# Performance work log

Measured on AMD Instinct MI355X. Metric: run time of the kernel, lower is better.

The kernel has to match this reference:

```python
import jax, jax.numpy as jnp
import numpy as np

W_LEN, BSZ, EMBED, NHEADS = 1024, 16, 512, 8
HEAD_DIM = EMBED // NHEADS
LN_EPS = 1e-5


def setup_inputs() -> dict:
    key = jax.random.key(0)
    ks = jax.random.split(key, 7)
    s = 1.0 / np.sqrt(EMBED)
    return {
        "feat": jax.random.normal(ks[0], (W_LEN, BSZ, EMBED), dtype=jnp.float32),
        "in_proj_w": jax.random.normal(ks[1], (3 * EMBED, EMBED), dtype=jnp.float32) * s,
        "in_proj_b": jax.random.normal(ks[2], (3 * EMBED,), dtype=jnp.float32) * 0.02,
        "out_w": jax.random.normal(ks[3], (EMBED, EMBED), dtype=jnp.float32) * s,
        "out_b": jax.random.normal(ks[4], (EMBED,), dtype=jnp.float32) * 0.02,
        "ln_g": jnp.ones((EMBED,), dtype=jnp.float32),
        "ln_b": jnp.zeros((EMBED,), dtype=jnp.float32),
    }


def _layernorm(x, g, b):
    mu = jnp.mean(x, axis=-1, keepdims=True)
    var = jnp.mean(jnp.square(x - mu), axis=-1, keepdims=True)
    return (x - mu) * jax.lax.rsqrt(var + LN_EPS) * g + b


def reference(feat, in_proj_w, in_proj_b, out_w, out_b, ln_g, ln_b):
    w, bsz, embed = feat.shape
    x = _layernorm(feat, ln_g, ln_b)
    # fused qkv projection (self-attention branch of the torch code)
    qkv = x @ in_proj_w.T + in_proj_b                      # [w, b, 3E]
    q, k, v = jnp.split(qkv, 3, axis=-1)
    scaling = float(HEAD_DIM) ** -0.5
    q = (q * scaling).reshape(w, bsz, NHEADS, HEAD_DIM)
    k = k.reshape(w, bsz, NHEADS, HEAD_DIM)
    v = v.reshape(w, bsz, NHEADS, HEAD_DIM)
    # scores [b, h, w, w2]
    attn = jnp.einsum('wnhd,vnhd->nhwv', q, k)
    attn = jax.nn.softmax(attn, axis=-1)
    v_out = jnp.einsum('nhwv,vnhd->wnhd', attn, v).reshape(w, bsz, embed)
    v_out = v_out @ out_w.T + out_b
    return feat + v_out
```

## Files before the change

### kernel.cpp

```cpp
#include <hip/hip_runtime.h>
#include <math.h>

#define W_LEN 1024
#define BSZ 16
#define EMBED 512
#define NHEADS 8
#define HEAD_DIM 64
#define TOKENS (W_LEN * BSZ)
#define LN_EPS 1e-5f

typedef __bf16 bf16_t;
typedef bf16_t bf16x8 __attribute__((ext_vector_type(8)));
typedef float f32x4 __attribute__((ext_vector_type(4)));

__device__ inline unsigned short f2bf(float f) {
    unsigned int u = __float_as_uint(f);
    u += 0x7fffu + ((u >> 16) & 1u);
    return (unsigned short)(u >> 16);
}

__device__ __forceinline__ void async16(const void* g, void* l) {
    __builtin_amdgcn_global_load_lds(
        (__attribute__((address_space(1))) void*)g,
        (__attribute__((address_space(3))) void*)l, 16, 0, 0);
}

__global__ __launch_bounds__(256) void cvt_f32_bf16(const float* __restrict__ src,
                                                    unsigned short* __restrict__ dst) {
    int i = (blockIdx.x * 256 + threadIdx.x) * 4;
    float4 f = *(const float4*)(src + i);
    uint2 p;
    p.x = (unsigned)f2bf(f.x) | ((unsigned)f2bf(f.y) << 16);
    p.y = (unsigned)f2bf(f.z) | ((unsigned)f2bf(f.w) << 16);
    *(uint2*)(dst + i) = p;
}

__global__ __launch_bounds__(256) void ln_kernel(
    const float* __restrict__ feat, const float* __restrict__ g,
    const float* __restrict__ b, unsigned short* __restrict__ xln)
{
    int tid   = threadIdx.x;
    int token = blockIdx.x * 4 + (tid >> 6);
    int lane  = tid & 63;
    const float* row = feat + (size_t)token * EMBED;

    float x[8];
    *(float4*)(x)     = *(const float4*)(row + lane * 4);
    *(float4*)(x + 4) = *(const float4*)(row + 256 + lane * 4);

    float sum = 0.f, ssq = 0.f;
#pragma unroll
    for (int i = 0; i < 8; i++) { sum += x[i]; ssq += x[i] * x[i]; }
#pragma unroll
    for (int off = 32; off > 0; off >>= 1) {
        sum += __shfl_xor(sum, off, 64);
        ssq += __shfl_xor(ssq, off, 64);
    }
    float mu  = sum * (1.0f / EMBED);
    float var = ssq * (1.0f / EMBED) - mu * mu;
    float rs  = rsqrtf(var + LN_EPS);

    float gg[8], bb[8], o[8];
    *(float4*)(gg)     = *(const float4*)(g + lane * 4);
    *(float4*)(gg + 4) = *(const float4*)(g + 256 + lane * 4);
    *(float4*)(bb)     = *(const float4*)(b + lane * 4);
    *(float4*)(bb + 4) = *(const float4*)(b + 256 + lane * 4);
#pragma unroll
    for (int i = 0; i < 8; i++) o[i] = (x[i] - mu) * rs * gg[i] + bb[i];

    unsigned short* orow = xln + (size_t)token * EMBED;
    uint2 lo, hi;
    lo.x = (unsigned)f2bf(o[0]) | ((unsigned)f2bf(o[1]) << 16);
    lo.y = (unsigned)f2bf(o[2]) | ((unsigned)f2bf(o[3]) << 16);
    hi.x = (unsigned)f2bf(o[4]) | ((unsigned)f2bf(o[5]) << 16);
    hi.y = (unsigned)f2bf(o[6]) | ((unsigned)f2bf(o[7]) << 16);
    *(uint2*)(orow + lane * 4)       = lo;
    *(uint2*)(orow + 256 + lane * 4) = hi;
}

__device__ __forceinline__ void gemm_core(const unsigned short* __restrict__ A,
                                          const unsigned short* __restrict__ Bt,
                                          int i0, int j0,
                                          unsigned short (*As0)[32], unsigned short (*As1)[32],
                                          unsigned short (*Bs0)[32], unsigned short (*Bs1)[32],
                                          f32x4 acc[4][4])
{
    int t = threadIdx.x;
    int wave = t >> 6, lane = t & 63, quad = lane >> 4, l16 = lane & 15;
    int wm = (wave >> 1) * 64, wn = (wave & 1) * 64;
    int srow = t >> 2, scol = (t & 3) * 8;
    const unsigned short* ga0 = A  + (size_t)(i0 + srow) * EMBED + scol;
    const unsigned short* ga1 = A  + (size_t)(i0 + srow + 64) * EMBED + scol;
    const unsigned short* gb0 = Bt + (size_t)(j0 + srow) * EMBED + scol;
    const unsigned short* gb1 = Bt + (size_t)(j0 + srow + 64) * EMBED + scol;

    for (int k0 = 0; k0 < EMBED; k0 += 64) {
        __syncthreads();
        async16(ga0 + k0,      &As0[srow][scol]);
        async16(ga1 + k0,      &As0[srow + 64][scol]);
        async16(gb0 + k0,      &Bs0[srow][scol]);
        async16(gb1 + k0,      &Bs0[srow + 64][scol]);
        async16(ga0 + k0 + 32, &As1[srow][scol]);
        async16(ga1 + k0 + 32, &As1[srow + 64][scol]);
        async16(gb0 + k0 + 32, &Bs1[srow][scol]);
        async16(gb1 + k0 + 32, &Bs1[srow + 64][scol]);
        __syncthreads();

#pragma unroll
        for (int h = 0; h < 2; h++) {
            unsigned short (*Ah)[32] = h ? As1 : As0;
            unsigned short (*Bh)[32] = h ? Bs1 : Bs0;
            bf16x8 af[4], bfr[4];
#pragma unroll
            for (int m = 0; m < 4; m++) af[m]  = *(const bf16x8*)&Ah[wm + m * 16 + l16][quad * 8];
#pragma unroll
            for (int n = 0; n < 4; n++) bfr[n] = *(const bf16x8*)&Bh[wn + n * 16 + l16][quad * 8];
#pragma unroll
            for (int m = 0; m < 4; m++)
#pragma unroll
                for (int n = 0; n < 4; n++)
                    acc[m][n] = __builtin_amdgcn_mfma_f32_16x16x32_bf16(af[m], bfr[n], acc[m][n], 0, 0, 0);
        }
    }
}

__global__ __launch_bounds__(256) void qkv_gemm_mfma(
    const unsigned short* __restrict__ A, const unsigned short* __restrict__ Bt,
    const float* __restrict__ bias, unsigned short* __restrict__ qo,
    unsigned short* __restrict__ ko, unsigned short* __restrict__ vo)
{
    __shared__ unsigned short As0[128][32], As1[128][32];
    __shared__ unsigned short Bs0[128][32], Bs1[128][32];
    f32x4 acc[4][4];
    const f32x4 z = {0.f, 0.f, 0.f, 0.f};
#pragma unroll
    for (int m = 0; m < 4; m++)
#pragma unroll
        for (int n = 0; n < 4; n++) acc[m][n] = z;

    int i0 = blockIdx.x * 128, j0 = blockIdx.y * 128;
    gemm_core(A, Bt, i0, j0, As0, As1, Bs0, Bs1, acc);

    int t = threadIdx.x, wave = t >> 6, lane = t & 63, quad = lane >> 4, l16 = lane & 15;
    int wm = (wave >> 1) * 64, wn = (wave & 1) * 64;
    int seg = j0 >> 9;
    unsigned short* outp = (seg == 0) ? qo : ((seg == 1) ? ko : vo);
    float scale = (seg == 0) ? 0.125f : 1.0f;

    float bj[4]; int hh[4], dd[4];
#pragma unroll
    for (int n = 0; n < 4; n++) {
        int j = j0 + wn + n * 16 + l16;
        bj[n] = bias[j];
        hh[n] = (j >> 6) & 7;
        dd[n] = j & 63;
    }
#pragma unroll
    for (int m = 0; m < 4; m++)
#pragma unroll
        for (int r = 0; r < 4; r++) {
            int token = i0 + wm + m * 16 + quad * 4 + r;
            int w  = token >> 4;
            int b_ = token & 15;
#pragma unroll
            for (int n = 0; n < 4; n++) {
                size_t idx = (((size_t)(b_ * NHEADS + hh[n]) * W_LEN + w) << 6) + dd[n];
                outp[idx] = f2bf((acc[m][n][r] + bj[n]) * scale);
            }
        }
}

__global__ __launch_bounds__(256) void out_gemm_mfma(
    const unsigned short* __restrict__ A, const unsigned short* __restrict__ Bt,
    const float* __restrict__ bias, const float* __restrict__ feat,
    float* __restrict__ out)
{
    __shared__ unsigned short As0[128][32], As1[128][32];
    __shared__ unsigned short Bs0[128][32], Bs1[128][32];
    f32x4 acc[4][4];
    const f32x4 z = {0.f, 0.f, 0.f, 0.f};
#pragma unroll
    for (int m = 0; m < 4; m++)
#pragma unroll
        for (int n = 0; n < 4; n++) acc[m][n] = z;

    int i0 = blockIdx.x * 128, j0 = blockIdx.y * 128;
    gemm_core(A, Bt, i0, j0, As0, As1, Bs0, Bs1, acc);

    int t = threadIdx.x, wave = t >> 6, lane = t & 63, quad = lane >> 4, l16 = lane & 15;
    int wm = (wave >> 1) * 64, wn = (wave & 1) * 64;

    float bj[4];
#pragma unroll
    for (int n = 0; n < 4; n++) bj[n] = bias[j0 + wn + n * 16 + l16];
#pragma unroll
    for (int m = 0; m < 4; m++)
#pragma unroll
        for (int r = 0; r < 4; r++) {
            int token = i0 + wm + m * 16 + quad * 4 + r;
#pragma unroll
            for (int n = 0; n < 4; n++) {
                int col = j0 + wn + n * 16 + l16;
                size_t idx = (size_t)token * EMBED + col;
                out[idx] = acc[m][n][r] + bj[n] + feat[idx];
            }
        }
}

__global__ __launch_bounds__(256, 4) void attn_mfma(
    const unsigned short* __restrict__ q, const unsigned short* __restrict__ k,
    const unsigned short* __restrict__ v, unsigned short* __restrict__ outp)
{
    __shared__ union {
        unsigned short Q[128][72];
        struct {
            unsigned short K[64][64];
            unsigned short V[64][72];
            unsigned short P[4][32][72];
        } s;
    } sm;

    int t = threadIdx.x, wave = t >> 6, lane = t & 63, quad = lane >> 4, l16 = lane & 15;
    int bh = blockIdx.x;
    int q0 = blockIdx.y * 128;
    const unsigned short* qp = q + ((size_t)bh * W_LEN + q0) * HEAD_DIM;
    const unsigned short* kp = k + (size_t)bh * W_LEN * HEAD_DIM;
    const unsigned short* vp = v + (size_t)bh * W_LEN * HEAD_DIM;

    {
        int qr = t >> 1, qc0 = (t & 1) * 32;
#pragma unroll
        for (int c = 0; c < 32; c += 8)
            *(uint4*)&sm.Q[qr][qc0 + c] = *(const uint4*)(qp + (size_t)qr * 64 + qc0 + c);
    }
    __syncthreads();
    bf16x8 qf[2][2];
#pragma unroll
    for (int nt = 0; nt < 2; nt++)
#pragma unroll
        for (int ks = 0; ks < 2; ks++)
            qf[nt][ks] = *(const bf16x8*)&sm.Q[wave * 32 + nt * 16 + l16][ks * 32 + quad * 8];
    __syncthreads();

    float l_st[2] = {0.f, 0.f};
    f32x4 o_acc[4][2];
    const f32x4 z = {0.f, 0.f, 0.f, 0.f};
#pragma unroll
    for (int m = 0; m < 4; m++)
#pragma unroll
        for (int n = 0; n < 2; n++) o_acc[m][n] = z;

    unsigned short* kl = &sm.s.K[0][0];
    int sr = t >> 3;
    int sc = ((t & 7) ^ (sr & 7)) * 8;
    int j2 = t & 31, vc = (t >> 5) * 8;

    uint4 kg[2];
    union { uint4 u; unsigned short sv[8]; } vg0, vg1;
#pragma unroll
    for (int j = 0; j < 2; j++)
        kg[j] = *(const uint4*)(kp + (size_t)(sr + j * 32) * 64 + sc);
    vg0.u = *(const uint4*)(vp + (size_t)(2 * j2) * 64 + vc);
    vg1.u = *(const uint4*)(vp + (size_t)(2 * j2 + 1) * 64 + vc);

    for (int kt = 0; kt < W_LEN; kt += 64) {
        __syncthreads();
#pragma unroll
        for (int j = 0; j < 2; j++)
            *(uint4*)(kl + (size_t)(t + j * 256) * 8) = kg[j];
#pragma unroll
        for (int i = 0; i < 8; i++) {
            unsigned int pk = (unsigned)vg0.sv[i] | ((unsigned)vg1.sv[i] << 16);
            *(unsigned int*)&sm.s.V[vc + i][2 * j2] = pk;
        }
        __syncthreads();

        int ktn = (kt + 64 < W_LEN) ? kt + 64 : kt;
#pragma unroll
        for (int j = 0; j < 2; j++)
            kg[j] = *(const uint4*)(kp + (size_t)(ktn + sr + j * 32) * 64 + sc);
        vg0.u = *(const uint4*)(vp + (size_t)(ktn + 2 * j2) * 64 + vc);
        vg1.u = *(const uint4*)(vp + (size_t)(ktn + 2 * j2 + 1) * 64 + vc);

        f32x4 s[4][2];
#pragma unroll
        for (int mt = 0; mt < 4; mt++)
#pragma unroll
            for (int nt = 0; nt < 2; nt++) s[mt][nt] = z;
#pragma unroll
        for (int ks = 0; ks < 2; ks++) {
            int swz = (((ks * 4 + quad) ^ (l16 & 7)) * 8);
            bf16x8 kf[4];
#pragma unroll
            for (int mt = 0; mt < 4; mt++)
                kf[mt] = *(const bf16x8*)(kl + (size_t)(mt * 16 + l16) * 64 + swz);
#pragma unroll
            for (int mt = 0; mt < 4; mt++)
#pragma unroll
                for (int nt = 0; nt < 2; nt++)
                    s[mt][nt] = __builtin_amdgcn_mfma_f32_16x16x32_bf16(kf[mt], qf[nt][ks], s[mt][nt], 0, 0, 0);
        }

#pragma unroll
        for (int nt = 0; nt < 2; nt++) {
            float sum = 0.f;
#pragma unroll
            for (int mt = 0; mt < 4; mt++)
#pragma unroll
                for (int r = 0; r < 4; r++) {
                    float p = __expf(s[mt][nt][r]);
                    s[mt][nt][r] = p;
                    sum += p;
                }
            sum += __shfl_xor(sum, 16, 64);
            sum += __shfl_xor(sum, 32, 64);
            l_st[nt] += sum;
        }

#pragma unroll
        for (int nt = 0; nt < 2; nt++)
#pragma unroll
            for (int mt = 0; mt < 4; mt++) {
                uint2 pk;
                pk.x = (unsigned)f2bf(s[mt][nt][0]) | ((unsigned)f2bf(s[mt][nt][1]) << 16);
                pk.y = (unsigned)f2bf(s[mt][nt][2]) | ((unsigned)f2bf(s[mt][nt][3]) << 16);
                *(uint2*)&sm.s.P[wave][nt * 16 + l16][mt * 16 + quad * 4] = pk;
            }
        asm volatile("s_waitcnt lgkmcnt(0)" ::: "memory");

#pragma unroll
        for (int ks = 0; ks < 2; ks++) {
            bf16x8 vf[4], pf[2];
#pragma unroll
            for (int mtd = 0; mtd < 4; mtd++)
                vf[mtd] = *(const bf16x8*)&sm.s.V[mtd * 16 + l16][ks * 32 + quad * 8];
#pragma unroll
            for (int nt = 0; nt < 2; nt++)
                pf[nt] = *(const bf16x8*)&sm.s.P[wave][nt * 16 + l16][ks * 32 + quad * 8];
#pragma unroll
            for (int mtd = 0; mtd < 4; mtd++)
#pragma unroll
                for (int nt = 0; nt < 2; nt++)
                    o_acc[mtd][nt] = __builtin_amdgcn_mfma_f32_16x16x32_bf16(vf[mtd], pf[nt], o_acc[mtd][nt], 0, 0, 0);
        }
    }

    int b_ = bh >> 3, h = bh & 7;
#pragma unroll
    for (int nt = 0; nt < 2; nt++) {
        int w = q0 + wave * 32 + nt * 16 + l16;
        int token = w * BSZ + b_;
        float inv = 1.0f / l_st[nt];
#pragma unroll
        for (int mtd = 0; mtd < 4; mtd++) {
            uint2 pk;
            pk.x = (unsigned)f2bf(o_acc[mtd][nt][0] * inv) |
                   ((unsigned)f2bf(o_acc[mtd][nt][1] * inv) << 16);
            pk.y = (unsigned)f2bf(o_acc[mtd][nt][2] * inv) |
                   ((unsigned)f2bf(o_acc[mtd][nt][3] * inv) << 16);
            *(uint2*)(outp + (size_t)token * EMBED + h * HEAD_DIM + mtd * 16 + quad * 4) = pk;
        }
    }
}

extern "C" void kernel_launch(void* const* d_in, const int* in_sizes, int n_in,
                              void* d_out, int out_size, void* d_ws, size_t ws_size,
                              hipStream_t stream) {
    const float* feat  = (const float*)d_in[0];
    const float* in_w  = (const float*)d_in[1];
    const float* in_b  = (const float*)d_in[2];
    const float* out_w = (const float*)d_in[3];
    const float* out_b = (const float*)d_in[4];
    const float* ln_g  = (const float*)d_in[5];
    const float* ln_b  = (const float*)d_in[6];
    float* out = (float*)d_out;

    char* ws = (char*)d_ws;
    const size_t SZB = (size_t)TOKENS * EMBED * sizeof(unsigned short);
    unsigned short* xln = (unsigned short*)ws;
    unsigned short* qb  = (unsigned short*)(ws + SZB);
    unsigned short* kb  = (unsigned short*)(ws + 2 * SZB);
    unsigned short* vb  = (unsigned short*)(ws + 3 * SZB);
    unsigned short* ao  = (unsigned short*)(ws + 4 * SZB);
    unsigned short* wib = (unsigned short*)(ws + 5 * SZB);
    unsigned short* wob = (unsigned short*)(ws + 5 * SZB +
                                            (size_t)3 * EMBED * EMBED * sizeof(unsigned short));

    cvt_f32_bf16<<<(3 * EMBED * EMBED) / 1024, 256, 0, stream>>>(in_w, wib);
    cvt_f32_bf16<<<(EMBED * EMBED) / 1024, 256, 0, stream>>>(out_w, wob);
    ln_kernel<<<TOKENS / 4, 256, 0, stream>>>(feat, ln_g, ln_b, xln);
    qkv_gemm_mfma<<<dim3(TOKENS / 128, (3 * EMBED) / 128), 256, 0, stream>>>(
        xln, wib, in_b, qb, kb, vb);
    attn_mfma<<<dim3(BSZ * NHEADS, W_LEN / 128), 256, 0, stream>>>(qb, kb, vb, ao);
    out_gemm_mfma<<<dim3(TOKENS / 128, EMBED / 128), 256, 0, stream>>>(
        ao, wob, out_b, feat, out);
}
```

Measured before the change: 218.5 us.

## Load K fragments directly to registers, use exp2 softmax, merge weight conversions

```diff
diff --git a/kernel.cpp b/kernel.cpp
--- a/kernel.cpp
+++ b/kernel.cpp
@@ -19,20 +19,30 @@
     return (unsigned short)(u >> 16);
 }
 
+__device__ __forceinline__ unsigned pkbf_trunc(float lo, float hi) {
+    return __builtin_amdgcn_perm(__float_as_uint(hi), __float_as_uint(lo), 0x07060302u);
+}
+
 __device__ __forceinline__ void async16(const void* g, void* l) {
     __builtin_amdgcn_global_load_lds(
         (__attribute__((address_space(1))) void*)g,
         (__attribute__((address_space(3))) void*)l, 16, 0, 0);
 }
 
-__global__ __launch_bounds__(256) void cvt_f32_bf16(const float* __restrict__ src,
-                                                    unsigned short* __restrict__ dst) {
+__global__ __launch_bounds__(256) void cvt_weights(const float* __restrict__ in_w,
+                                                   const float* __restrict__ out_w,
+                                                   unsigned short* __restrict__ wib,
+                                                   unsigned short* __restrict__ wob) {
+    const int N1 = 3 * EMBED * EMBED;
     int i = (blockIdx.x * 256 + threadIdx.x) * 4;
-    float4 f = *(const float4*)(src + i);
+    const float* src; unsigned short* dst; int off;
+    if (i < N1) { src = in_w;  dst = wib; off = i; }
+    else        { src = out_w; dst = wob; off = i - N1; }
+    float4 f = *(const float4*)(src + off);
     uint2 p;
     p.x = (unsigned)f2bf(f.x) | ((unsigned)f2bf(f.y) << 16);
     p.y = (unsigned)f2bf(f.z) | ((unsigned)f2bf(f.w) << 16);
-    *(uint2*)(dst + i) = p;
+    *(uint2*)(dst + off) = p;
 }
 
 __global__ __launch_bounds__(256) void ln_kernel(
@@ -145,7 +155,7 @@
     int wm = (wave >> 1) * 64, wn = (wave & 1) * 64;
     int seg = j0 >> 9;
     unsigned short* outp = (seg == 0) ? qo : ((seg == 1) ? ko : vo);
-    float scale = (seg == 0) ? 0.125f : 1.0f;
+    float scale = (seg == 0) ? 0.18033688f : 1.0f;
 
     float bj[4]; int hh[4], dd[4];
 #pragma unroll
@@ -214,7 +224,6 @@
     __shared__ union {
         unsigned short Q[128][72];
         struct {
-            unsigned short K[64][64];
             unsigned short V[64][72];
             unsigned short P[4][32][72];
         } s;
@@ -250,35 +259,32 @@
 #pragma unroll
         for (int n = 0; n < 2; n++) o_acc[m][n] = z;
 
-    unsigned short* kl = &sm.s.K[0][0];
-    int sr = t >> 3;
-    int sc = ((t & 7) ^ (sr & 7)) * 8;
+    const unsigned short* kfp = kp + (size_t)l16 * HEAD_DIM + quad * 8;
+
+    bf16x8 kf[4][2];
+#pragma unroll
+    for (int mt = 0; mt < 4; mt++)
+#pragma unroll
+        for (int ks = 0; ks < 2; ks++)
+            kf[mt][ks] = *(const bf16x8*)(kfp + (size_t)mt * 16 * HEAD_DIM + ks * 32);
+
     int j2 = t & 31, vc = (t >> 5) * 8;
-
-    uint4 kg[2];
-    union { uint4 u; unsigned short sv[8]; } vg0, vg1;
-#pragma unroll
-    for (int j = 0; j < 2; j++)
-        kg[j] = *(const uint4*)(kp + (size_t)(sr + j * 32) * 64 + sc);
+    union { uint4 u; unsigned w[4]; } vg0, vg1;
     vg0.u = *(const uint4*)(vp + (size_t)(2 * j2) * 64 + vc);
     vg1.u = *(const uint4*)(vp + (size_t)(2 * j2 + 1) * 64 + vc);
 
     for (int kt = 0; kt < W_LEN; kt += 64) {
         __syncthreads();
 #pragma unroll
-        for (int j = 0; j < 2; j++)
-            *(uint4*)(kl + (size_t)(t + j * 256) * 8) = kg[j];
-#pragma unroll
-        for (int i = 0; i < 8; i++) {
-            unsigned int pk = (unsigned)vg0.sv[i] | ((unsigned)vg1.sv[i] << 16);
-            *(unsigned int*)&sm.s.V[vc + i][2 * j2] = pk;
+        for (int w2 = 0; w2 < 4; w2++) {
+            unsigned lo = __builtin_amdgcn_perm(vg1.w[w2], vg0.w[w2], 0x05040100u);
+            unsigned hi = __builtin_amdgcn_perm(vg1.w[w2], vg0.w[w2], 0x07060302u);
+            *(unsigned*)&sm.s.V[vc + 2 * w2][2 * j2]     = lo;
+            *(unsigned*)&sm.s.V[vc + 2 * w2 + 1][2 * j2] = hi;
         }
         __syncthreads();
 
         int ktn = (kt + 64 < W_LEN) ? kt + 64 : kt;
-#pragma unroll
-        for (int j = 0; j < 2; j++)
-            kg[j] = *(const uint4*)(kp + (size_t)(ktn + sr + j * 32) * 64 + sc);
         vg0.u = *(const uint4*)(vp + (size_t)(ktn + 2 * j2) * 64 + vc);
         vg1.u = *(const uint4*)(vp + (size_t)(ktn + 2 * j2 + 1) * 64 + vc);
 
@@ -288,17 +294,20 @@
 #pragma unroll
             for (int nt = 0; nt < 2; nt++) s[mt][nt] = z;
 #pragma unroll
-        for (int ks = 0; ks < 2; ks++) {
-            int swz = (((ks * 4 + quad) ^ (l16 & 7)) * 8);
-            bf16x8 kf[4];
+        for (int ks = 0; ks < 2; ks++)
 #pragma unroll
             for (int mt = 0; mt < 4; mt++)
-                kf[mt] = *(const bf16x8*)(kl + (size_t)(mt * 16 + l16) * 64 + swz);
+#pragma unroll
+                for (int nt = 0; nt < 2; nt++)
+                    s[mt][nt] = __builtin_amdgcn_mfma_f32_16x16x32_bf16(kf[mt][ks], qf[nt][ks], s[mt][nt], 0, 0, 0);
+
+        {
+            const unsigned short* kfn = kfp + (size_t)ktn * HEAD_DIM;
 #pragma unroll
             for (int mt = 0; mt < 4; mt++)
 #pragma unroll
-                for (int nt = 0; nt < 2; nt++)
-                    s[mt][nt] = __builtin_amdgcn_mfma_f32_16x16x32_bf16(kf[mt], qf[nt][ks], s[mt][nt], 0, 0, 0);
+                for (int ks = 0; ks < 2; ks++)
+                    kf[mt][ks] = *(const bf16x8*)(kfn + (size_t)mt * 16 * HEAD_DIM + ks * 32);
         }
 
 #pragma unroll
@@ -308,7 +317,7 @@
             for (int mt = 0; mt < 4; mt++)
 #pragma unroll
                 for (int r = 0; r < 4; r++) {
-                    float p = __expf(s[mt][nt][r]);
+                    float p = exp2f(s[mt][nt][r]);
                     s[mt][nt][r] = p;
                     sum += p;
                 }
@@ -322,8 +331,8 @@
 #pragma unroll
             for (int mt = 0; mt < 4; mt++) {
                 uint2 pk;
-                pk.x = (unsigned)f2bf(s[mt][nt][0]) | ((unsigned)f2bf(s[mt][nt][1]) << 16);
-                pk.y = (unsigned)f2bf(s[mt][nt][2]) | ((unsigned)f2bf(s[mt][nt][3]) << 16);
+                pk.x = pkbf_trunc(s[mt][nt][0], s[mt][nt][1]);
+                pk.y = pkbf_trunc(s[mt][nt][2], s[mt][nt][3]);
                 *(uint2*)&sm.s.P[wave][nt * 16 + l16][mt * 16 + quad * 4] = pk;
             }
         asm volatile("s_waitcnt lgkmcnt(0)" ::: "memory");
@@ -354,10 +363,8 @@
 #pragma unroll
         for (int mtd = 0; mtd < 4; mtd++) {
             uint2 pk;
-            pk.x = (unsigned)f2bf(o_acc[mtd][nt][0] * inv) |
-                   ((unsigned)f2bf(o_acc[mtd][nt][1] * inv) << 16);
-            pk.y = (unsigned)f2bf(o_acc[mtd][nt][2] * inv) |
-                   ((unsigned)f2bf(o_acc[mtd][nt][3] * inv) << 16);
+            pk.x = pkbf_trunc(o_acc[mtd][nt][0] * inv, o_acc[mtd][nt][1] * inv);
+            pk.y = pkbf_trunc(o_acc[mtd][nt][2] * inv, o_acc[mtd][nt][3] * inv);
             *(uint2*)(outp + (size_t)token * EMBED + h * HEAD_DIM + mtd * 16 + quad * 4) = pk;
         }
     }
@@ -386,8 +393,7 @@
     unsigned short* wob = (unsigned short*)(ws + 5 * SZB +
                                             (size_t)3 * EMBED * EMBED * sizeof(unsigned short));
 
-    cvt_f32_bf16<<<(3 * EMBED * EMBED) / 1024, 256, 0, stream>>>(in_w, wib);
-    cvt_f32_bf16<<<(EMBED * EMBED) / 1024, 256, 0, stream>>>(out_w, wob);
+    cvt_weights<<<(4 * EMBED * EMBED) / 1024, 256, 0, stream>>>(in_w, out_w, wib, wob);
     ln_kernel<<<TOKENS / 4, 256, 0, stream>>>(feat, ln_g, ln_b, xln);
     qkv_gemm_mfma<<<dim3(TOKENS / 128, (3 * EMBED) / 128), 256, 0, stream>>>(
         xln, wib, in_b, qb, kb, vb);
```

After: 295.0 us. 35.0% more time.
